# Optimization experiments

Measured on AMD Instinct MI355X. Metric: run time of the kernel, lower is better.

The kernel has to match this reference:

```python
import jax, jax.numpy as jnp
import numpy as np
import math

B, T, D, H = 4, 2048, 1024, 16
DH = D // H


def setup_inputs() -> dict:
    key = jax.random.key(0)
    k1, k2, k3 = jax.random.split(key, 3)
    x = jax.random.normal(k1, (B, T, D), dtype=jnp.float32)
    # causal mask: True = masked (positions j > i)
    attn_mask = jnp.triu(jnp.ones((T, T), dtype=bool), k=1)
    key_padding_mask = jnp.zeros((B, T), dtype=bool)  # no padding
    W_qkv = jax.random.normal(k2, (D, 3 * D), dtype=jnp.float32) / math.sqrt(D)
    W_out = jax.random.normal(k3, (D, D), dtype=jnp.float32) / math.sqrt(D)
    return {"x": x, "W_qkv": W_qkv, "W_out": W_out,
            "attn_mask": attn_mask, "key_padding_mask": key_padding_mask}


def reference(x, W_qkv, W_out, attn_mask, key_padding_mask):
    # qkv projection (bias=False)
    qkv = x @ W_qkv                                   # [B,T,3D]
    q, k, v = jnp.split(qkv, 3, axis=-1)              # each [B,T,D]
    # reshape to heads: [B,H,T,DH]
    q = q.reshape(B, T, H, DH).transpose(0, 2, 1, 3)
    k = k.reshape(B, T, H, DH).transpose(0, 2, 1, 3)
    v = v.reshape(B, T, H, DH).transpose(0, 2, 1, 3)
    scale = 1.0 / math.sqrt(DH)
    scores = jnp.einsum('bhqd,bhkd->bhqk', q, k) * scale   # [B,H,T,T]
    neg_inf = jnp.float32(-jnp.inf)
    scores = jnp.where(attn_mask[None, None, :, :], neg_inf, scores)
    scores = jnp.where(key_padding_mask[:, None, None, :], neg_inf, scores)
    attn = jax.nn.softmax(scores, axis=-1)            # dropout p=0.0 -> identity
    out = jnp.einsum('bhqk,bhkd->bhqd', attn, v)      # [B,H,T,DH]
    out = out.transpose(0, 2, 1, 3).reshape(B, T, D)
    return out @ W_out
```

## Files before the change

kernel.cpp:

```cpp
#include <hip/hip_runtime.h>
#include <hip/hip_bf16.h>

#define Bsz 4
#define T 2048
#define D 1024
#define H 16
#define DH 64

typedef unsigned short u16;
typedef __attribute__((ext_vector_type(8))) __bf16 bf16x8;
typedef __attribute__((ext_vector_type(4))) float f32x4;

__device__ inline u16 f2bf(float f) {
  union { float f; unsigned u; } v; v.f = f;
  unsigned r = (v.u + 0x7FFFu + ((v.u >> 16) & 1u)) >> 16;
  return (u16)r;
}
__device__ inline unsigned pack_bf16(float a, float b) {
  union { float f; unsigned u; } A, B; A.f = a; B.f = b;
  unsigned au = A.u + 0x8000u, bu = B.u + 0x8000u;
  return __builtin_amdgcn_perm(bu, au, 0x07060302);
}

__device__ inline void gll16(const u16* g, u16* l) {
  __builtin_amdgcn_global_load_lds((const __attribute__((address_space(1))) void*)g,
                                   (__attribute__((address_space(3))) void*)l, 16, 0, 0);
}

__global__ __launch_bounds__(256) void convert_f32_bf16(const float* __restrict__ in,
                                                        u16* __restrict__ out, int n4) {
  int i = blockIdx.x * 256 + threadIdx.x;
  if (i < n4) {
    float4 v = reinterpret_cast<const float4*>(in)[i];
    ushort4 o;
    o.x = f2bf(v.x); o.y = f2bf(v.y); o.z = f2bf(v.z); o.w = f2bf(v.w);
    reinterpret_cast<ushort4*>(out)[i] = o;
  }
}

__global__ __launch_bounds__(256) void transpose_f32_bf16(const float* __restrict__ in,
                                                          u16* __restrict__ out, int K, int N) {
  __shared__ float tile[32][33];
  int tx = threadIdx.x & 31, ty = threadIdx.x >> 5;
  int n0 = blockIdx.x * 32, k0 = blockIdx.y * 32;
  #pragma unroll
  for (int i = 0; i < 4; ++i)
    tile[ty + i * 8][tx] = in[(size_t)(k0 + ty + i * 8) * N + n0 + tx];
  __syncthreads();
  #pragma unroll
  for (int i = 0; i < 4; ++i)
    out[(size_t)(n0 + ty + i * 8) * K + k0 + tx] = f2bf(tile[tx][ty + i * 8]);
}

template <int MODE>
__global__ __launch_bounds__(256) void gemm128(const u16* __restrict__ A, const u16* __restrict__ BT,
                                               float* __restrict__ C,
                                               u16* __restrict__ Qh, u16* __restrict__ Kh,
                                               u16* __restrict__ VTh, int M, int N, int K) {
  __shared__ u16 As[128][32];
  __shared__ u16 Bs[128][32];
  int tid = threadIdx.x;
  int m0 = blockIdx.y * 128, n0 = blockIdx.x * 128;
  int w = tid >> 6, lane = tid & 63;
  int llo = lane & 15, lhi = lane >> 4;
  int wm = (w >> 1) * 64, wn = (w & 1) * 64;

  f32x4 acc[4][4];
  #pragma unroll
  for (int i = 0; i < 4; ++i)
    #pragma unroll
    for (int j = 0; j < 4; ++j) acc[i][j] = (f32x4){0.f, 0.f, 0.f, 0.f};

  const u16* gA = A + (size_t)(m0 + w * 32 + (lane >> 2)) * K + (lane & 3) * 8;
  const u16* gB = BT + (size_t)(n0 + w * 32 + (lane >> 2)) * K + (lane & 3) * 8;

  for (int k0 = 0; k0 < K; k0 += 32) {
    gll16(gA + k0, &As[w * 32][0]);
    gll16(gA + (size_t)16 * K + k0, &As[w * 32 + 16][0]);
    gll16(gB + k0, &Bs[w * 32][0]);
    gll16(gB + (size_t)16 * K + k0, &Bs[w * 32 + 16][0]);
    __syncthreads();
    bf16x8 af[4], bfr[4];
    #pragma unroll
    for (int i = 0; i < 4; ++i)
      af[i] = *reinterpret_cast<const bf16x8*>(&As[wm + i * 16 + llo][lhi * 8]);
    #pragma unroll
    for (int j = 0; j < 4; ++j)
      bfr[j] = *reinterpret_cast<const bf16x8*>(&Bs[wn + j * 16 + llo][lhi * 8]);
    #pragma unroll
    for (int i = 0; i < 4; ++i)
      #pragma unroll
      for (int j = 0; j < 4; ++j)
        acc[i][j] = __builtin_amdgcn_mfma_f32_16x16x32_bf16(af[i], bfr[j], acc[i][j], 0, 0, 0);
    __syncthreads();
  }

  if (MODE == 0) {
    #pragma unroll
    for (int i = 0; i < 4; ++i)
      #pragma unroll
      for (int j = 0; j < 4; ++j) {
        int nl = n0 + wn + j * 16 + llo;
        #pragma unroll
        for (int r = 0; r < 4; ++r) {
          int ml = m0 + wm + i * 16 + lhi * 4 + r;
          C[(size_t)ml * N + nl] = acc[i][j][r];
        }
      }
  } else {
    int seg = n0 >> 10;
    #pragma unroll
    for (int i = 0; i < 4; ++i) {
      int mbase = m0 + wm + i * 16 + lhi * 4;
      int t0 = mbase & (T - 1);
      int b_ = mbase >> 11;
      #pragma unroll
      for (int j = 0; j < 4; ++j) {
        int nl = n0 + wn + j * 16 + llo;
        int h = (nl >> 6) & 15, d = nl & 63;
        int bh = b_ * H + h;
        if (seg == 0) {
          #pragma unroll
          for (int r = 0; r < 4; ++r)
            Qh[((size_t)bh * T + t0 + r) * DH + d] = f2bf(acc[i][j][r] * 0.125f);
        } else if (seg == 1) {
          #pragma unroll
          for (int r = 0; r < 4; ++r)
            Kh[((size_t)bh * T + t0 + r) * DH + d] = f2bf(acc[i][j][r]);
        } else {
          uint2 p;
          p.x = pack_bf16(acc[i][j][0], acc[i][j][1]);
          p.y = pack_bf16(acc[i][j][2], acc[i][j][3]);
          *reinterpret_cast<uint2*>(&VTh[((size_t)bh * DH + d) * T + t0]) = p;
        }
      }
    }
  }
}

__global__ __launch_bounds__(1024, 4) void attn_fwd(const u16* __restrict__ Qh, const u16* __restrict__ Kh,
                                                    const u16* __restrict__ VTh, u16* __restrict__ AO) {
  __shared__ u16 QP[16][16][72];
  __shared__ u16 Ks[64][72];
  __shared__ u16 Vs[64][72];
  int tid = threadIdx.x;
  int qp = blockIdx.x, bh = blockIdx.y;
  int w = tid >> 6, lane = tid & 63;
  int llo = lane & 15, lhi = lane >> 4;

  int qrow_s = tid >> 2, qc = tid & 3;
  int krow_s = tid >> 4, kc = tid & 15;
  const u16* kbase = Kh + ((size_t)bh * T + krow_s) * DH + kc * 4;
  const u16* vbase = VTh + ((size_t)bh * DH + krow_s) * T + kc * 4;
  int b = bh >> 4, h = bh & 15;

  #pragma unroll 1
  for (int half = 0; half < 2; ++half) {
    int qt = half ? (7 - qp) : qp;
    int q0 = qt * 256;

    bf16x8 aq[2];
    {
      const uint4* g = reinterpret_cast<const uint4*>(
          Qh + ((size_t)bh * T + q0 + qrow_s) * DH + qc * 16);
      uint4 a = g[0], bb = g[1];
      uint4* dst = reinterpret_cast<uint4*>(&QP[w][qrow_s & 15][qc * 16]);
      dst[0] = a; dst[1] = bb;
      #pragma unroll
      for (int ks = 0; ks < 2; ++ks)
        aq[ks] = *reinterpret_cast<const bf16x8*>(&QP[w][llo][ks * 32 + lhi * 8]);
    }

    f32x4 o[4];
    #pragma unroll
    for (int i = 0; i < 4; ++i) o[i] = (f32x4){0.f, 0.f, 0.f, 0.f};
    float l_run = 0.f;

    int nj = 4 * qt + 4;
    uint2 ka = *reinterpret_cast<const uint2*>(kbase);
    uint2 va = *reinterpret_cast<const uint2*>(vbase);

    #pragma unroll 1
    for (int j = 0; j < nj; ++j) {
      __syncthreads();
      *reinterpret_cast<uint2*>(&Ks[krow_s][kc * 4]) = ka;
      *reinterpret_cast<uint2*>(&Vs[krow_s][kc * 4]) = va;
      if (j + 1 < nj) {
        ka = *reinterpret_cast<const uint2*>(kbase + (size_t)(j + 1) * 64 * DH);
        va = *reinterpret_cast<const uint2*>(vbase + (j + 1) * 64);
      } else if (half == 0) {
        ka = *reinterpret_cast<const uint2*>(kbase);
        va = *reinterpret_cast<const uint2*>(vbase);
      }
      __syncthreads();

      if (q0 + w * 16 + 15 >= j * 64) {
        f32x4 sc[4];
        #pragma unroll
        for (int kt = 0; kt < 4; ++kt) {
          bf16x8 bk0 = *reinterpret_cast<const bf16x8*>(&Ks[kt * 16 + llo][lhi * 8]);
          bf16x8 bk1 = *reinterpret_cast<const bf16x8*>(&Ks[kt * 16 + llo][32 + lhi * 8]);
          f32x4 z = (f32x4){0.f, 0.f, 0.f, 0.f};
          f32x4 t0 = __builtin_amdgcn_mfma_f32_16x16x32_bf16(bk0, aq[0], z, 0, 0, 0);
          sc[kt] = __builtin_amdgcn_mfma_f32_16x16x32_bf16(bk1, aq[1], t0, 0, 0, 0);
        }

        if (j >= 4 * qt) {
          int qrow_g = q0 + w * 16 + llo;
          #pragma unroll
          for (int kt = 0; kt < 4; ++kt)
            #pragma unroll
            for (int r = 0; r < 4; ++r) {
              int key_g = j * 64 + kt * 16 + lhi * 4 + r;
              if (key_g > qrow_g) sc[kt][r] = -__builtin_inff();
            }
        }

        float s_sum = 0.f;
        #pragma unroll
        for (int kt = 0; kt < 4; ++kt)
          #pragma unroll
          for (int r = 0; r < 4; ++r) {
            float p = __expf(sc[kt][r]);
            sc[kt][r] = p;
            s_sum += p;
          }
        s_sum += __shfl_xor(s_sum, 16);
        s_sum += __shfl_xor(s_sum, 32);
        l_run += s_sum;

        #pragma unroll
        for (int kt = 0; kt < 4; ++kt) {
          uint2 p;
          p.x = pack_bf16(sc[kt][0], sc[kt][1]);
          p.y = pack_bf16(sc[kt][2], sc[kt][3]);
          *reinterpret_cast<uint2*>(&QP[w][llo][kt * 16 + lhi * 4]) = p;
        }

        #pragma unroll
        for (int kk2 = 0; kk2 < 2; ++kk2) {
          bf16x8 pa = *reinterpret_cast<const bf16x8*>(&QP[w][llo][kk2 * 32 + lhi * 8]);
          #pragma unroll
          for (int nt = 0; nt < 4; ++nt) {
            bf16x8 bv = *reinterpret_cast<const bf16x8*>(&Vs[nt * 16 + llo][kk2 * 32 + lhi * 8]);
            o[nt] = __builtin_amdgcn_mfma_f32_16x16x32_bf16(pa, bv, o[nt], 0, 0, 0);
          }
        }
      }
    }

    #pragma unroll
    for (int r = 0; r < 4; ++r) {
      float inv = 1.f / __shfl(l_run, lhi * 4 + r);
      int t = q0 + w * 16 + lhi * 4 + r;
      #pragma unroll
      for (int nt = 0; nt < 4; ++nt)
        AO[((size_t)(b * T + t)) * D + h * 64 + nt * 16 + llo] = f2bf(o[nt][r] * inv);
    }
  }
}

extern "C" void kernel_launch(void* const* d_in, const int* in_sizes, int n_in,
                              void* d_out, int out_size, void* d_ws, size_t ws_size,
                              hipStream_t stream) {
  (void)in_sizes; (void)n_in; (void)out_size;
  const float* x = (const float*)d_in[0];
  const float* Wqkv = (const float*)d_in[1];
  const float* Wout = (const float*)d_in[2];
  float* out = (float*)d_out;

  char* ws = (char*)d_ws;
  size_t off = 0;
  u16* xb = (u16*)(ws + off);    off += (size_t)Bsz * T * D * 2;
  u16* WqkvT = (u16*)(ws + off); off += (size_t)3 * D * D * 2;
  u16* WoutT = (u16*)(ws + off); off += (size_t)D * D * 2;
  u16* Qh = (u16*)(ws + off);    off += (size_t)Bsz * H * T * DH * 2;
  u16* Kh = (u16*)(ws + off);    off += (size_t)Bsz * H * T * DH * 2;
  u16* VTh = (u16*)(ws + off);   off += (size_t)Bsz * H * DH * T * 2;
  u16* AO = xb;
  if (ws_size < off) return;

  int n4 = Bsz * T * D / 4;
  convert_f32_bf16<<<(n4 + 255) / 256, 256, 0, stream>>>(x, xb, n4);
  transpose_f32_bf16<<<dim3(3 * D / 32, D / 32), 256, 0, stream>>>(Wqkv, WqkvT, D, 3 * D);
  transpose_f32_bf16<<<dim3(D / 32, D / 32), 256, 0, stream>>>(Wout, WoutT, D, D);
  gemm128<1><<<dim3(3 * D / 128, Bsz * T / 128), 256, 0, stream>>>(xb, WqkvT, nullptr, Qh, Kh, VTh,
                                                                   Bsz * T, 3 * D, D);
  attn_fwd<<<dim3(4, Bsz * H), 1024, 0, stream>>>(Qh, Kh, VTh, AO);
  gemm128<0><<<dim3(D / 128, Bsz * T / 128), 256, 0, stream>>>(AO, WoutT, out, nullptr, nullptr, nullptr,
                                                               Bsz * T, D, D);
}
```

Measured before the change: 281.7 us.

## Double-buffer GEMMs with swizzled LDS, XCD-aware block remap, and finer attention tiles

Replaces the GEMM with a 512-thread, double-buffered kernel that stages the next K-slice while computing the current one. It uses XOR-swizzled LDS layouts to avoid bank conflicts, remaps block IDs across the eight XCDs for L2 locality, and sets MFMA priority. The QKV GEMM uses a 128x192 tile. Attention moves to 512-thread blocks over 128-row query tiles, with swizzled, unpadded LDS and 16-byte K/V loads, which doubles grid parallelism. The changes add complexity and depend on exact swizzle correctness, and smaller attention tiles reload K/V more often.

```diff
diff --git a/kernel.cpp b/kernel.cpp
--- a/kernel.cpp
+++ b/kernel.cpp
@@ -52,71 +52,111 @@
     out[(size_t)(n0 + ty + i * 8) * K + k0 + tx] = f2bf(tile[tx][ty + i * 8]);
 }
 
-template <int MODE>
-__global__ __launch_bounds__(256) void gemm128(const u16* __restrict__ A, const u16* __restrict__ BT,
-                                               float* __restrict__ C,
-                                               u16* __restrict__ Qh, u16* __restrict__ Kh,
-                                               u16* __restrict__ VTh, int M, int N, int K) {
-  __shared__ u16 As[128][32];
-  __shared__ u16 Bs[128][32];
+template <int BN, int MODE>
+__global__ __launch_bounds__(512, 4) void gemmX(const u16* __restrict__ A, const u16* __restrict__ BT,
+                                                float* __restrict__ C,
+                                                u16* __restrict__ Qh, u16* __restrict__ Kh,
+                                                u16* __restrict__ VTh, int M, int N, int K) {
+  constexpr int NB = BN / 64;
+  __shared__ alignas(16) u16 SA[2][2][128][32];
+  __shared__ alignas(16) u16 SB[2][2][BN][32];
+  u16* sbFlat = &SB[0][0][0][0];
   int tid = threadIdx.x;
-  int m0 = blockIdx.y * 128, n0 = blockIdx.x * 128;
+
+  int flat = blockIdx.y * gridDim.x + blockIdx.x;
+  int cpx = (int)(gridDim.x * gridDim.y) >> 3;
+  int nf = (flat & 7) * cpx + (flat >> 3);
+  int bx = nf % (int)gridDim.x, by = nf / (int)gridDim.x;
+  int m0 = by * 128, n0 = bx * BN;
+
   int w = tid >> 6, lane = tid & 63;
   int llo = lane & 15, lhi = lane >> 4;
-  int wm = (w >> 1) * 64, wn = (w & 1) * 64;
-
-  f32x4 acc[4][4];
+  int wr = w >> 2, wc = w & 3;
+
+  int cs = ((lhi ^ ((llo >> 1) & 3)) << 3);
+
+  int rA = w * 16 + (lane >> 2);
+  const u16* srcA = A + (size_t)(m0 + rA) * K + (((lane & 3) ^ ((rA >> 1) & 3)) << 3);
+  const u16* srcB[NB];
+  #pragma unroll
+  for (int q = 0; q < NB; ++q) {
+    int rr = q * 128 + w * 16 + (lane >> 2);
+    int kB = (rr >= BN) ? 1 : 0;
+    int rB = rr - kB * BN;
+    srcB[q] = BT + (size_t)(n0 + rB) * K + kB * 32 + (((lane & 3) ^ ((rB >> 1) & 3)) << 3);
+  }
+
+  f32x4 acc[4][NB];
   #pragma unroll
   for (int i = 0; i < 4; ++i)
     #pragma unroll
-    for (int j = 0; j < 4; ++j) acc[i][j] = (f32x4){0.f, 0.f, 0.f, 0.f};
-
-  const u16* gA = A + (size_t)(m0 + w * 32 + (lane >> 2)) * K + (lane & 3) * 8;
-  const u16* gB = BT + (size_t)(n0 + w * 32 + (lane >> 2)) * K + (lane & 3) * 8;
-
-  for (int k0 = 0; k0 < K; k0 += 32) {
-    gll16(gA + k0, &As[w * 32][0]);
-    gll16(gA + (size_t)16 * K + k0, &As[w * 32 + 16][0]);
-    gll16(gB + k0, &Bs[w * 32][0]);
-    gll16(gB + (size_t)16 * K + k0, &Bs[w * 32 + 16][0]);
-    __syncthreads();
-    bf16x8 af[4], bfr[4];
-    #pragma unroll
-    for (int i = 0; i < 4; ++i)
-      af[i] = *reinterpret_cast<const bf16x8*>(&As[wm + i * 16 + llo][lhi * 8]);
-    #pragma unroll
-    for (int j = 0; j < 4; ++j)
-      bfr[j] = *reinterpret_cast<const bf16x8*>(&Bs[wn + j * 16 + llo][lhi * 8]);
-    #pragma unroll
-    for (int i = 0; i < 4; ++i)
-      #pragma unroll
-      for (int j = 0; j < 4; ++j)
-        acc[i][j] = __builtin_amdgcn_mfma_f32_16x16x32_bf16(af[i], bfr[j], acc[i][j], 0, 0, 0);
-    __syncthreads();
+    for (int j = 0; j < NB; ++j) acc[i][j] = (f32x4){0.f, 0.f, 0.f, 0.f};
+
+  int nt = K >> 6;
+
+  auto stage = [&](int g, int buf) {
+    #pragma unroll
+    for (int k = 0; k < 2; ++k)
+      gll16(srcA + g * 64 + k * 32, &SA[buf][k][w * 16][0]);
+    #pragma unroll
+    for (int q = 0; q < NB; ++q)
+      gll16(srcB[q] + g * 64, sbFlat + (size_t)buf * (2 * BN * 32) + (q * 128 + w * 16) * 32);
+  };
+
+  stage(0, 0);
+  asm volatile("s_waitcnt vmcnt(0)" ::: "memory");
+  __builtin_amdgcn_s_barrier();
+
+  #pragma unroll 2
+  for (int g = 0; g < nt; ++g) {
+    int p = g & 1;
+    if (g + 1 < nt) stage(g + 1, 1 - p);
+
+    #pragma unroll
+    for (int k = 0; k < 2; ++k) {
+      bf16x8 aA[4], bB[NB];
+      #pragma unroll
+      for (int i = 0; i < 4; ++i)
+        aA[i] = *reinterpret_cast<const bf16x8*>(&SA[p][k][wr * 64 + i * 16 + llo][cs]);
+      #pragma unroll
+      for (int j = 0; j < NB; ++j)
+        bB[j] = *reinterpret_cast<const bf16x8*>(&SB[p][k][wc * (BN / 4) + j * 16 + llo][cs]);
+      __builtin_amdgcn_s_setprio(1);
+      #pragma unroll
+      for (int i = 0; i < 4; ++i)
+        #pragma unroll
+        for (int j = 0; j < NB; ++j)
+          acc[i][j] = __builtin_amdgcn_mfma_f32_16x16x32_bf16(aA[i], bB[j], acc[i][j], 0, 0, 0);
+      __builtin_amdgcn_s_setprio(0);
+    }
+
+    asm volatile("s_waitcnt vmcnt(0)" ::: "memory");
+    __builtin_amdgcn_s_barrier();
   }
 
   if (MODE == 0) {
     #pragma unroll
-    for (int i = 0; i < 4; ++i)
-      #pragma unroll
-      for (int j = 0; j < 4; ++j) {
-        int nl = n0 + wn + j * 16 + llo;
-        #pragma unroll
-        for (int r = 0; r < 4; ++r) {
-          int ml = m0 + wm + i * 16 + lhi * 4 + r;
-          C[(size_t)ml * N + nl] = acc[i][j][r];
-        }
+    for (int i = 0; i < 4; ++i) {
+      int ml = m0 + wr * 64 + i * 16 + lhi * 4;
+      #pragma unroll
+      for (int j = 0; j < NB; ++j) {
+        int nl = n0 + wc * (BN / 4) + j * 16 + llo;
+        #pragma unroll
+        for (int r = 0; r < 4; ++r)
+          C[(size_t)(ml + r) * N + nl] = acc[i][j][r];
       }
+    }
   } else {
-    int seg = n0 >> 10;
     #pragma unroll
     for (int i = 0; i < 4; ++i) {
-      int mbase = m0 + wm + i * 16 + lhi * 4;
+      int mbase = m0 + wr * 64 + i * 16 + lhi * 4;
       int t0 = mbase & (T - 1);
       int b_ = mbase >> 11;
       #pragma unroll
-      for (int j = 0; j < 4; ++j) {
-        int nl = n0 + wn + j * 16 + llo;
+      for (int j = 0; j < NB; ++j) {
+        int ncol0 = n0 + wc * (BN / 4) + j * 16;
+        int seg = ncol0 >> 10;
+        int nl = ncol0 + llo;
         int h = (nl >> 6) & 15, d = nl & 63;
         int bh = b_ * H + h;
         if (seg == 0) {
@@ -128,47 +168,50 @@
           for (int r = 0; r < 4; ++r)
             Kh[((size_t)bh * T + t0 + r) * DH + d] = f2bf(acc[i][j][r]);
         } else {
-          uint2 p;
-          p.x = pack_bf16(acc[i][j][0], acc[i][j][1]);
-          p.y = pack_bf16(acc[i][j][2], acc[i][j][3]);
-          *reinterpret_cast<uint2*>(&VTh[((size_t)bh * DH + d) * T + t0]) = p;
+          uint2 pk;
+          pk.x = pack_bf16(acc[i][j][0], acc[i][j][1]);
+          pk.y = pack_bf16(acc[i][j][2], acc[i][j][3]);
+          *reinterpret_cast<uint2*>(&VTh[((size_t)bh * DH + d) * T + t0]) = pk;
         }
       }
     }
   }
 }
 
-__global__ __launch_bounds__(1024, 4) void attn_fwd(const u16* __restrict__ Qh, const u16* __restrict__ Kh,
-                                                    const u16* __restrict__ VTh, u16* __restrict__ AO) {
-  __shared__ u16 QP[16][16][72];
-  __shared__ u16 Ks[64][72];
-  __shared__ u16 Vs[64][72];
+__global__ __launch_bounds__(512, 4) void attn_fwd(const u16* __restrict__ Qh, const u16* __restrict__ Kh,
+                                                   const u16* __restrict__ VTh, u16* __restrict__ AO) {
+  __shared__ u16 QP[8][16][64];
+  __shared__ u16 Ks[64][64];
+  __shared__ u16 Vs[64][64];
   int tid = threadIdx.x;
   int qp = blockIdx.x, bh = blockIdx.y;
   int w = tid >> 6, lane = tid & 63;
   int llo = lane & 15, lhi = lane >> 4;
+  int swz = llo & 7;
 
   int qrow_s = tid >> 2, qc = tid & 3;
-  int krow_s = tid >> 4, kc = tid & 15;
-  const u16* kbase = Kh + ((size_t)bh * T + krow_s) * DH + kc * 4;
-  const u16* vbase = VTh + ((size_t)bh * DH + krow_s) * T + kc * 4;
+  int krow_s = tid >> 3, kc = tid & 7;
+  int kvcol = ((kc ^ (krow_s & 7)) << 3);
+  const u16* kbase = Kh + ((size_t)bh * T + krow_s) * DH + kc * 8;
+  const u16* vbase = VTh + ((size_t)bh * DH + krow_s) * T + kc * 8;
   int b = bh >> 4, h = bh & 15;
 
   #pragma unroll 1
   for (int half = 0; half < 2; ++half) {
-    int qt = half ? (7 - qp) : qp;
-    int q0 = qt * 256;
+    int qt = half ? (15 - qp) : qp;
+    int q0 = qt * 128;
 
     bf16x8 aq[2];
     {
       const uint4* g = reinterpret_cast<const uint4*>(
           Qh + ((size_t)bh * T + q0 + qrow_s) * DH + qc * 16);
       uint4 a = g[0], bb = g[1];
-      uint4* dst = reinterpret_cast<uint4*>(&QP[w][qrow_s & 15][qc * 16]);
-      dst[0] = a; dst[1] = bb;
+      int r7 = qrow_s & 7;
+      *reinterpret_cast<uint4*>(&QP[w][qrow_s & 15][((2 * qc) ^ r7) << 3]) = a;
+      *reinterpret_cast<uint4*>(&QP[w][qrow_s & 15][((2 * qc + 1) ^ r7) << 3]) = bb;
       #pragma unroll
       for (int ks = 0; ks < 2; ++ks)
-        aq[ks] = *reinterpret_cast<const bf16x8*>(&QP[w][llo][ks * 32 + lhi * 8]);
+        aq[ks] = *reinterpret_cast<const bf16x8*>(&QP[w][llo][((ks * 4 + lhi) ^ swz) << 3]);
     }
 
     f32x4 o[4];
@@ -176,21 +219,21 @@
     for (int i = 0; i < 4; ++i) o[i] = (f32x4){0.f, 0.f, 0.f, 0.f};
     float l_run = 0.f;
 
-    int nj = 4 * qt + 4;
-    uint2 ka = *reinterpret_cast<const uint2*>(kbase);
-    uint2 va = *reinterpret_cast<const uint2*>(vbase);
+    int nj = 2 * qt + 2;
+    uint4 ka = *reinterpret_cast<const uint4*>(kbase);
+    uint4 va = *reinterpret_cast<const uint4*>(vbase);
 
     #pragma unroll 1
     for (int j = 0; j < nj; ++j) {
       __syncthreads();
-      *reinterpret_cast<uint2*>(&Ks[krow_s][kc * 4]) = ka;
-      *reinterpret_cast<uint2*>(&Vs[krow_s][kc * 4]) = va;
+      *reinterpret_cast<uint4*>(&Ks[krow_s][kvcol]) = ka;
+      *reinterpret_cast<uint4*>(&Vs[krow_s][kvcol]) = va;
       if (j + 1 < nj) {
-        ka = *reinterpret_cast<const uint2*>(kbase + (size_t)(j + 1) * 64 * DH);
-        va = *reinterpret_cast<const uint2*>(vbase + (j + 1) * 64);
+        ka = *reinterpret_cast<const uint4*>(kbase + (size_t)(j + 1) * 64 * DH);
+        va = *reinterpret_cast<const uint4*>(vbase + (j + 1) * 64);
       } else if (half == 0) {
-        ka = *reinterpret_cast<const uint2*>(kbase);
-        va = *reinterpret_cast<const uint2*>(vbase);
+        ka = *reinterpret_cast<const uint4*>(kbase);
+        va = *reinterpret_cast<const uint4*>(vbase);
       }
       __syncthreads();
 
@@ -198,14 +241,14 @@
         f32x4 sc[4];
         #pragma unroll
         for (int kt = 0; kt < 4; ++kt) {
-          bf16x8 bk0 = *reinterpret_cast<const bf16x8*>(&Ks[kt * 16 + llo][lhi * 8]);
-          bf16x8 bk1 = *reinterpret_cast<const bf16x8*>(&Ks[kt * 16 + llo][32 + lhi * 8]);
+          bf16x8 bk0 = *reinterpret_cast<const bf16x8*>(&Ks[kt * 16 + llo][(lhi ^ swz) << 3]);
+          bf16x8 bk1 = *reinterpret_cast<const bf16x8*>(&Ks[kt * 16 + llo][((4 + lhi) ^ swz) << 3]);
           f32x4 z = (f32x4){0.f, 0.f, 0.f, 0.f};
           f32x4 t0 = __builtin_amdgcn_mfma_f32_16x16x32_bf16(bk0, aq[0], z, 0, 0, 0);
           sc[kt] = __builtin_amdgcn_mfma_f32_16x16x32_bf16(bk1, aq[1], t0, 0, 0, 0);
         }
 
-        if (j >= 4 * qt) {
+        if (j >= 2 * qt) {
           int qrow_g = q0 + w * 16 + llo;
           #pragma unroll
           for (int kt = 0; kt < 4; ++kt)
@@ -234,15 +277,16 @@
           uint2 p;
           p.x = pack_bf16(sc[kt][0], sc[kt][1]);
           p.y = pack_bf16(sc[kt][2], sc[kt][3]);
-          *reinterpret_cast<uint2*>(&QP[w][llo][kt * 16 + lhi * 4]) = p;
+          *reinterpret_cast<uint2*>(
+              &QP[w][llo][(((2 * kt + (lhi >> 1)) ^ swz) << 3) + (lhi & 1) * 4]) = p;
         }
 
         #pragma unroll
         for (int kk2 = 0; kk2 < 2; ++kk2) {
-          bf16x8 pa = *reinterpret_cast<const bf16x8*>(&QP[w][llo][kk2 * 32 + lhi * 8]);
+          bf16x8 pa = *reinterpret_cast<const bf16x8*>(&QP[w][llo][((kk2 * 4 + lhi) ^ swz) << 3]);
           #pragma unroll
           for (int nt = 0; nt < 4; ++nt) {
-            bf16x8 bv = *reinterpret_cast<const bf16x8*>(&Vs[nt * 16 + llo][kk2 * 32 + lhi * 8]);
+            bf16x8 bv = *reinterpret_cast<const bf16x8*>(&Vs[nt * 16 + llo][((kk2 * 4 + lhi) ^ swz) << 3]);
             o[nt] = __builtin_amdgcn_mfma_f32_16x16x32_bf16(pa, bv, o[nt], 0, 0, 0);
           }
         }
@@ -284,9 +328,9 @@
   convert_f32_bf16<<<(n4 + 255) / 256, 256, 0, stream>>>(x, xb, n4);
   transpose_f32_bf16<<<dim3(3 * D / 32, D / 32), 256, 0, stream>>>(Wqkv, WqkvT, D, 3 * D);
   transpose_f32_bf16<<<dim3(D / 32, D / 32), 256, 0, stream>>>(Wout, WoutT, D, D);
-  gemm128<1><<<dim3(3 * D / 128, Bsz * T / 128), 256, 0, stream>>>(xb, WqkvT, nullptr, Qh, Kh, VTh,
-                                                                   Bsz * T, 3 * D, D);
-  attn_fwd<<<dim3(4, Bsz * H), 1024, 0, stream>>>(Qh, Kh, VTh, AO);
-  gemm128<0><<<dim3(D / 128, Bsz * T / 128), 256, 0, stream>>>(AO, WoutT, out, nullptr, nullptr, nullptr,
-                                                               Bsz * T, D, D);
-}
+  gemmX<192, 1><<<dim3(3 * D / 192, Bsz * T / 128), 512, 0, stream>>>(xb, WqkvT, nullptr, Qh, Kh, VTh,
+                                                                      Bsz * T, 3 * D, D);
+  attn_fwd<<<dim3(8, Bsz * H), 512, 0, stream>>>(Qh, Kh, VTh, AO);
+  gemmX<128, 0><<<dim3(D / 128, Bsz * T / 128), 512, 0, stream>>>(AO, WoutT, out, nullptr, nullptr, nullptr,
+                                                                  Bsz * T, D, D);
+}
```

Measured after the change: 242.0 us. 14.1% less time.
